# Performance work log

Hardware: AMD Instinct MI355X
Metric: run time of the kernel (lower is better)

Reference implementation:

```python
import math
import jax, jax.numpy as jnp
import numpy as np


def setup_inputs() -> dict:
    key = jax.random.key(0)
    k1, k2 = jax.random.split(key)
    x = jax.random.normal(k1, (32, 3, 64, 64), dtype=jnp.float32)   # (B,C,H,W)
    y = jax.random.normal(k2, (512, 3, 64, 64), dtype=jnp.float32)  # (N,C,H,W)
    return {"x": x, "y": y}


def reference(x, y):
    # Faithful to torch rfft/irfft with normalized=True (unitary / 'ortho' scaling).
    B, C, H, W = x.shape
    scale = math.sqrt(H * W)  # self.N in the torch module
    X = jnp.fft.rfft2(x, norm="ortho")  # (B,C,H,W//2+1) complex
    Y = jnp.fft.rfft2(y, norm="ortho")  # (N,C,H,W//2+1) complex
    # conj(X) . Y summed over channels, fused as one complex contraction
    G = jnp.einsum("bchw,nchw->bnhw", jnp.conj(X), Y)  # (B,N,H,W//2+1)
    g = jnp.fft.irfft2(G, s=(H, W), norm="ortho") * scale  # (B,N,H,W)
    m = jnp.max(g, axis=(-2, -1))  # MaxPool2d(kernel=input_size) -> (B,N)
    xx = jnp.linalg.norm(x.reshape(B, -1), axis=-1)[:, None]  # (B,1)
    yy = jnp.linalg.norm(y.reshape(y.shape[0], -1), axis=-1)[None, :]  # (1,N)
    return m / xx / yy
```

## Files before the change

kernel.cpp:

```cpp
#include <hip/hip_runtime.h>
#include <math.h>

#define FBINS 2112
#define CSC 66

typedef float cplx __attribute__((ext_vector_type(2)));
typedef __fp16 half2v __attribute__((ext_vector_type(2)));
#define MK2(a,b) (cplx){(float)(a), (float)(b)}

__device__ __forceinline__ cplx shufxy(cplx a){ return __builtin_shufflevector(a, a, 1, 0); }
template<int S> __device__ __forceinline__ cplx imul(cplx a){
    return (S > 0) ? shufxy(a) * MK2(-1.f, 1.f) : shufxy(a) * MK2(1.f, -1.f);
}
template<int S> __device__ __forceinline__ cplx cmul_tw(cplx a, cplx w){
    cplx ws = shufxy(w);
    return (S > 0) ? a.x*w + a.y*(ws*MK2(-1.f, 1.f))
                   : a.x*(w*MK2(1.f, -1.f)) + a.y*ws;
}

__device__ __forceinline__ unsigned pack16(float a, float b){
    half2v h = __builtin_amdgcn_cvt_pkrtz(a, b);
    return __builtin_bit_cast(unsigned, h);
}
__device__ __forceinline__ half2v h2(unsigned u){ return __builtin_bit_cast(half2v, u); }
__device__ __forceinline__ float fdot2(half2v a, half2v b, float c){
#if __has_builtin(__builtin_amdgcn_fdot2)
    return __builtin_amdgcn_fdot2(a, b, c, false);
#else
    return c + (float)a.x*(float)b.x + (float)a.y*(float)b.y;
#endif
}
__device__ __forceinline__ void dotw(unsigned ux, unsigned uy, float& r, float& s){
    unsigned ys = ((uy >> 16) | (uy << 16)) ^ 0x80000000u;
    r = fdot2(h2(ux), h2(uy), r);
    s = fdot2(h2(ux), h2(ys), s);
}

template<int S>
__device__ __forceinline__ void dft8(cplx v[8]) {
    const float C = 0.70710678118654752440f;
    cplx t0=v[0]+v[4], t4=v[0]-v[4];
    cplx t1=v[1]+v[5], t5=v[1]-v[5];
    cplx t2=v[2]+v[6], t6=v[2]-v[6];
    cplx t3=v[3]+v[7], t7=v[3]-v[7];
    cplx u0=t0+t2, u2=t0-t2;
    cplx u1=t1+t3, u3=t1-t3;
    v[0]=u0+u1; v[4]=u0-u1;
    cplx m3=imul<S>(u3);
    v[2]=u2+m3; v[6]=u2-m3;
    cplx z0=t4;
    cplx z1 = C*(t5 + imul<S>(t5));
    cplx z2 = imul<S>(t6);
    cplx z3 = C*(imul<S>(t7) - t7);
    cplx w0=z0+z2, w2=z0-z2;
    cplx w1=z1+z3, w3=z1-z3;
    v[1]=w0+w1; v[5]=w0-w1;
    cplx mb=imul<S>(w3);
    v[3]=w2+mb; v[7]=w2-mb;
}

template<int S>
__device__ __forceinline__ void fft64_from_regs(
    cplx v[8], cplx* __restrict__ mem, int base, int j, const cplx wj[7])
{
    dft8<S>(v);
    #pragma unroll
    for (int k=1;k<8;++k) v[k] = cmul_tw<S>(v[k], wj[k-1]);
    #pragma unroll
    for (int k=0;k<8;++k) mem[base + 8*j + (k^j)] = v[k];
    #pragma unroll
    for (int n=0;n<8;++n) v[n] = mem[base + 8*n + (j^n)];
    dft8<S>(v);
}

__device__ __forceinline__ void init_twtable(cplx* TWS, int tid){
    if (tid < 56) {
        int jj = tid / 7, kk = tid - 7*jj + 1;
        float sn, cs;
        sincosf(6.283185307179586f * (float)(jj*kk) / 64.0f, &sn, &cs);
        TWS[tid] = MK2(cs, sn);
    }
}
__device__ __forceinline__ void load_tw(const cplx* TWS, int j, cplx wj[7]){
    #pragma unroll
    for (int k=0;k<7;++k) wj[k] = TWS[j*7+k];
}

__global__ __launch_bounds__(256) void fwd_fft_kernel(
    const float* __restrict__ in, unsigned* __restrict__ o,
    float* __restrict__ pn)
{
    __shared__ __align__(16) cplx CL[2176];
    __shared__ cplx TWS[56];
    __shared__ float red[4];
    const int tid = threadIdx.x, G = tid>>3, j = tid&7;

    init_twtable(TWS, tid);

    const float* img = in + (size_t)blockIdx.x * 4096;

    cplx wj[7];
    {
        cplx v[8];
        float ns = 0.f;
        #pragma unroll
        for (int nn=0;nn<8;++nn){ int w=8*nn+j;
            float a = img[64*G + w], c = img[64*(G+32) + w];
            v[nn] = MK2(a, c);
            ns = fmaf(a, a, ns); ns = fmaf(c, c, ns); }
        #pragma unroll
        for (int off = 32; off; off >>= 1) ns += __shfl_xor(ns, off);
        if ((tid & 63) == 0) red[tid >> 6] = ns;
        __syncthreads();
        load_tw(TWS, j, wj);
        int base = CSC*G;
        fft64_from_regs<-1>(v, CL, base, j, wj);
        #pragma unroll
        for (int k=0;k<8;++k) CL[base + j + 8*k] = v[k];
    }
    __syncthreads();

    {
        cplx v[8];
        if (G == 0) {
            #pragma unroll
            for (int nn=0;nn<8;++nn){
                int r=8*nn+j, p=r&31, hi=r>>5;
                cplx a0  = CL[CSC*p + 0];
                cplx a32 = CL[CSC*p + 32];
                v[nn] = hi ? MK2(a0.y, a32.y) : MK2(a0.x, a32.x);
            }
        } else {
            const int c = G;
            #pragma unroll
            for (int nn=0;nn<8;++nn){
                int r=8*nn+j, p=r&31, hi=r>>5;
                cplx A  = CL[CSC*p + c];
                cplx Bm = CL[CSC*p + 64 - c];
                if (!hi) v[nn] = 0.5f*(A + Bm*MK2(1.f,-1.f));
                else     v[nn] = 0.5f*(shufxy(A)*MK2(1.f,-1.f) + shufxy(Bm));
            }
        }
        __syncthreads();
        int base = CSC*G;
        fft64_from_regs<-1>(v, CL, base, j, wj);
        #pragma unroll
        for (int k=0;k<8;++k) CL[base + j + 8*k] = v[k];
    }
    __syncthreads();

    unsigned* a = o + (size_t)blockIdx.x * FBINS;
    for (int i = tid; i < FBINS; i += 256) {
        int wp = i>>6, h = i&63;
        cplx r;
        if (wp == 0) {
            int h2i = (64-h)&63;
            cplx av = CL[h], bb = CL[h2i];
            r = 0.5f*(av + bb*MK2(1.f,-1.f));
        } else if (wp == 32) {
            int h2i = (64-h)&63;
            cplx av = CL[h], bb = CL[h2i];
            r = 0.5f*(shufxy(av)*MK2(1.f,-1.f) + shufxy(bb));
        } else {
            r = CL[CSC*wp + h];
        }
        a[i] = pack16(r.x, r.y);
    }
    if (tid == 0) pn[blockIdx.x] = red[0] + red[1] + red[2] + red[3];
}

__global__ __launch_bounds__(256) void corr_kernel(
    const unsigned* __restrict__ Xh, const unsigned* __restrict__ Yh,
    const float* __restrict__ px, const float* __restrict__ py,
    float* __restrict__ out)
{
    __shared__ __align__(16) cplx CL[2176];
    __shared__ cplx TWS[56];
    __shared__ float red[4];
    const int tid = threadIdx.x, G = tid>>3, j = tid&7;

    const int blk = blockIdx.x;
    const int xcd = blk & 7, idx = blk >> 3;
    const int n = xcd*64 + (idx & 63);
    const int b = idx >> 6;

    init_twtable(TWS, tid);

    const float x2 = px[3*b] + px[3*b+1] + px[3*b+2];
    const float y2 = py[3*n] + py[3*n+1] + py[3*n+2];
    const float dinv = rsqrtf(x2 * y2) * (1.0f/4096.0f);

    const uint4* pX = (const uint4*)Xh + (size_t)b * 3 * 528;
    const uint4* pY = (const uint4*)Yh + (size_t)n * 3 * 528;
    #pragma unroll
    for (int t = 0; t < 3; ++t) {
        int i = tid + (t<<8);
        if (i < 528) {
            float r[4], s[4];
            #pragma unroll
            for (int k=0;k<4;++k){ r[k]=0.f; s[k]=0.f; }
            #pragma unroll
            for (int ch = 0; ch < 3; ++ch) {
                uint4 ux = pX[ch*528 + i];
                uint4 uy = pY[ch*528 + i];
                dotw(ux.x, uy.x, r[0], s[0]);
                dotw(ux.y, uy.y, r[1], s[1]);
                dotw(ux.z, uy.z, r[2], s[2]);
                dotw(ux.w, uy.w, r[3], s[3]);
            }
            int bin = 4*i;
            int sI = CSC*(bin>>6) + (bin&63);
            *(float4*)&CL[sI]   = make_float4(r[0],s[0],r[1],s[1]);
            *(float4*)&CL[sI+2] = make_float4(r[2],s[2],r[3],s[3]);
        }
    }
    __syncthreads();

    cplx wj[7]; load_tw(TWS, j, wj);

    {
        cplx v[8];
        if (G == 0) {
            #pragma unroll
            for (int nn=0;nn<8;++nn){
                int h = 8*nn + j;
                cplx a = CL[h];
                cplx c = CL[CSC*32 + h];
                v[nn] = a + imul<1>(c);
            }
        } else {
            #pragma unroll
            for (int nn=0;nn<8;++nn) v[nn] = CL[CSC*G + 8*nn + j];
        }
        fft64_from_regs<1>(v, CL, CSC*G, j, wj);
        #pragma unroll
        for (int k=0;k<4;++k)
            *(float4*)&CL[CSC*G + 2*(j+8*k)] =
                make_float4(v[k].x, v[k].y, v[k+4].x, v[k+4].y);
    }
    __syncthreads();

    float m = -3.4e38f;
    {
        cplx v[8];
        if (j == 0) {
            float4 f = *(float4*)&CL[2*G];
            v[0] = MK2(f.x, f.z);
            v[4] = MK2(f.y, f.w);
        } else {
            float4 f = *(float4*)&CL[CSC*j + 2*G];
            v[0] = MK2(f.x,f.y) + imul<1>(MK2(f.z,f.w));
            float4 g2 = *(float4*)&CL[CSC*(32-j) + 2*G];
            v[4] = MK2(g2.x,g2.y)*MK2(1.f,-1.f) + shufxy(MK2(g2.z,g2.w));
        }
        #pragma unroll
        for (int nn=1;nn<4;++nn){
            int w = 8*nn + j;
            float4 f = *(float4*)&CL[CSC*w + 2*G];
            v[nn] = MK2(f.x,f.y) + imul<1>(MK2(f.z,f.w));
        }
        #pragma unroll
        for (int nn=5;nn<8;++nn){
            int w2 = 64 - (8*nn + j);
            float4 f = *(float4*)&CL[CSC*w2 + 2*G];
            v[nn] = MK2(f.x,f.y)*MK2(1.f,-1.f) + shufxy(MK2(f.z,f.w));
        }
        __syncthreads();
        fft64_from_regs<1>(v, CL, CSC*G, j, wj);
        #pragma unroll
        for (int k=0;k<8;++k) m = fmaxf(m, fmaxf(v[k].x, v[k].y));
    }
    #pragma unroll
    for (int off = 32; off; off >>= 1) m = fmaxf(m, __shfl_xor(m, off));
    if ((tid & 63) == 0) red[tid >> 6] = m;
    __syncthreads();
    if (tid == 0) {
        float mm = fmaxf(fmaxf(red[0], red[1]), fmaxf(red[2], red[3]));
        out[b*512 + n] = mm * dinv;
    }
}

extern "C" void kernel_launch(void* const* d_in, const int* in_sizes, int n_in,
                              void* d_out, int out_size, void* d_ws, size_t ws_size,
                              hipStream_t stream) {
    const float* x = (const float*)d_in[0];
    const float* y = (const float*)d_in[1];
    float* out = (float*)d_out;

    unsigned* Xh = (unsigned*)d_ws;
    unsigned* Yh = Xh + 96 * FBINS;
    float* px = (float*)(Yh + 1536 * FBINS);
    float* py = px + 96;

    fwd_fft_kernel<<<96,   256, 0, stream>>>(x, Xh, px);
    fwd_fft_kernel<<<1536, 256, 0, stream>>>(y, Yh, py);
    corr_kernel<<<16384, 256, 0, stream>>>(Xh, Yh, px, py, out);
}
```

Before: 94.95 us.

## Permute spectrum layout so correlation products load directly into FFT registers

The forward FFT now writes each row's frequency bins in a transposed slot order, so each corr_kernel thread can load its 8 bins for the first inverse FFT stage straight from global memory. The channel dot products are accumulated in registers, which removes the shared-memory store, a __syncthreads and a reload. The Nyquist-column fold for row group 0 is done inline. Twiddle factors now come from a __constant__ table instead of being computed with sincosf into shared memory, which drops one more barrier in each kernel.

```diff
diff --git a/kernel.cpp b/kernel.cpp
--- a/kernel.cpp
+++ b/kernel.cpp
@@ -34,6 +34,40 @@
     unsigned ys = ((uy >> 16) | (uy << 16)) ^ 0x80000000u;
     r = fdot2(h2(ux), h2(uy), r);
     s = fdot2(h2(ux), h2(ys), s);
+}
+__device__ __forceinline__ void dotw_i(unsigned ux, unsigned uy, cplx& v){
+    float rr = 0.f, ss = 0.f;
+    dotw(ux, uy, rr, ss);
+    v += MK2(-ss, rr);
+}
+
+__device__ __constant__ float TWC[112] = {
+  1.f,0.f, 1.f,0.f, 1.f,0.f, 1.f,0.f, 1.f,0.f, 1.f,0.f, 1.f,0.f,
+  0.9951847267f,0.0980171403f, 0.9807852804f,0.1950903220f, 0.9569403357f,0.2902846773f,
+  0.9238795325f,0.3826834324f, 0.8819212643f,0.4713967368f, 0.8314696123f,0.5555702330f,
+  0.7730104534f,0.6343932842f,
+  0.9807852804f,0.1950903220f, 0.9238795325f,0.3826834324f, 0.8314696123f,0.5555702330f,
+  0.7071067812f,0.7071067812f, 0.5555702330f,0.8314696123f, 0.3826834324f,0.9238795325f,
+  0.1950903220f,0.9807852804f,
+  0.9569403357f,0.2902846773f, 0.8314696123f,0.5555702330f, 0.6343932842f,0.7730104534f,
+  0.3826834324f,0.9238795325f, 0.0980171403f,0.9951847267f, -0.1950903220f,0.9807852804f,
+  -0.4713967368f,0.8819212643f,
+  0.9238795325f,0.3826834324f, 0.7071067812f,0.7071067812f, 0.3826834324f,0.9238795325f,
+  0.f,1.f, -0.3826834324f,0.9238795325f, -0.7071067812f,0.7071067812f,
+  -0.9238795325f,0.3826834324f,
+  0.8819212643f,0.4713967368f, 0.5555702330f,0.8314696123f, 0.0980171403f,0.9951847267f,
+  -0.3826834324f,0.9238795325f, -0.7730104534f,0.6343932842f, -0.9807852804f,0.1950903220f,
+  -0.9569403357f,-0.2902846773f,
+  0.8314696123f,0.5555702330f, 0.3826834324f,0.9238795325f, -0.1950903220f,0.9807852804f,
+  -0.7071067812f,0.7071067812f, -0.9807852804f,0.1950903220f, -0.9238795325f,-0.3826834324f,
+  -0.5555702330f,-0.8314696123f,
+  0.7730104534f,0.6343932842f, 0.1950903220f,0.9807852804f, -0.4713967368f,0.8819212643f,
+  -0.9238795325f,0.3826834324f, -0.9569403357f,-0.2902846773f, -0.5555702330f,-0.8314696123f,
+  0.0980171403f,-0.9951847267f
+};
+__device__ __forceinline__ void load_tw(int j, cplx wj[7]){
+    #pragma unroll
+    for (int k=0;k<7;++k) wj[k] = MK2(TWC[(j*7+k)*2], TWC[(j*7+k)*2+1]);
 }
 
 template<int S>
@@ -73,33 +107,17 @@
     dft8<S>(v);
 }
 
-__device__ __forceinline__ void init_twtable(cplx* TWS, int tid){
-    if (tid < 56) {
-        int jj = tid / 7, kk = tid - 7*jj + 1;
-        float sn, cs;
-        sincosf(6.283185307179586f * (float)(jj*kk) / 64.0f, &sn, &cs);
-        TWS[tid] = MK2(cs, sn);
-    }
-}
-__device__ __forceinline__ void load_tw(const cplx* TWS, int j, cplx wj[7]){
-    #pragma unroll
-    for (int k=0;k<7;++k) wj[k] = TWS[j*7+k];
-}
-
 __global__ __launch_bounds__(256) void fwd_fft_kernel(
     const float* __restrict__ in, unsigned* __restrict__ o,
     float* __restrict__ pn)
 {
     __shared__ __align__(16) cplx CL[2176];
-    __shared__ cplx TWS[56];
     __shared__ float red[4];
     const int tid = threadIdx.x, G = tid>>3, j = tid&7;
 
-    init_twtable(TWS, tid);
-
+    cplx wj[7]; load_tw(j, wj);
     const float* img = in + (size_t)blockIdx.x * 4096;
 
-    cplx wj[7];
     {
         cplx v[8];
         float ns = 0.f;
@@ -111,8 +129,6 @@
         #pragma unroll
         for (int off = 32; off; off >>= 1) ns += __shfl_xor(ns, off);
         if ((tid & 63) == 0) red[tid >> 6] = ns;
-        __syncthreads();
-        load_tw(TWS, j, wj);
         int base = CSC*G;
         fft64_from_regs<-1>(v, CL, base, j, wj);
         #pragma unroll
@@ -164,7 +180,8 @@
         } else {
             r = CL[CSC*wp + h];
         }
-        a[i] = pack16(r.x, r.y);
+        int slot = ((h & 7) << 3) | (h >> 3);
+        a[(wp << 6) | slot] = pack16(r.x, r.y);
     }
     if (tid == 0) pn[blockIdx.x] = red[0] + red[1] + red[2] + red[3];
 }
@@ -175,7 +192,6 @@
     float* __restrict__ out)
 {
     __shared__ __align__(16) cplx CL[2176];
-    __shared__ cplx TWS[56];
     __shared__ float red[4];
     const int tid = threadIdx.x, G = tid>>3, j = tid&7;
 
@@ -184,65 +200,54 @@
     const int n = xcd*64 + (idx & 63);
     const int b = idx >> 6;
 
-    init_twtable(TWS, tid);
-
     const float x2 = px[3*b] + px[3*b+1] + px[3*b+2];
     const float y2 = py[3*n] + py[3*n+1] + py[3*n+2];
     const float dinv = rsqrtf(x2 * y2) * (1.0f/4096.0f);
 
-    const uint4* pX = (const uint4*)Xh + (size_t)b * 3 * 528;
-    const uint4* pY = (const uint4*)Yh + (size_t)n * 3 * 528;
-    #pragma unroll
-    for (int t = 0; t < 3; ++t) {
-        int i = tid + (t<<8);
-        if (i < 528) {
-            float r[4], s[4];
-            #pragma unroll
-            for (int k=0;k<4;++k){ r[k]=0.f; s[k]=0.f; }
-            #pragma unroll
-            for (int ch = 0; ch < 3; ++ch) {
-                uint4 ux = pX[ch*528 + i];
-                uint4 uy = pY[ch*528 + i];
-                dotw(ux.x, uy.x, r[0], s[0]);
-                dotw(ux.y, uy.y, r[1], s[1]);
-                dotw(ux.z, uy.z, r[2], s[2]);
-                dotw(ux.w, uy.w, r[3], s[3]);
-            }
-            int bin = 4*i;
-            int sI = CSC*(bin>>6) + (bin&63);
-            *(float4*)&CL[sI]   = make_float4(r[0],s[0],r[1],s[1]);
-            *(float4*)&CL[sI+2] = make_float4(r[2],s[2],r[3],s[3]);
-        }
-    }
-    __syncthreads();
-
-    cplx wj[7]; load_tw(TWS, j, wj);
-
+    const uint4* pX4 = (const uint4*)Xh + (size_t)b * 3 * 528;
+    const uint4* pY4 = (const uint4*)Yh + (size_t)n * 3 * 528;
+    cplx v[8];
     {
-        cplx v[8];
-        if (G == 0) {
-            #pragma unroll
-            for (int nn=0;nn<8;++nn){
-                int h = 8*nn + j;
-                cplx a = CL[h];
-                cplx c = CL[CSC*32 + h];
-                v[nn] = a + imul<1>(c);
-            }
-        } else {
-            #pragma unroll
-            for (int nn=0;nn<8;++nn) v[nn] = CL[CSC*G + 8*nn + j];
-        }
-        fft64_from_regs<1>(v, CL, CSC*G, j, wj);
-        #pragma unroll
-        for (int k=0;k<4;++k)
-            *(float4*)&CL[CSC*G + 2*(j+8*k)] =
-                make_float4(v[k].x, v[k].y, v[k+4].x, v[k+4].y);
-    }
+        float r[8], s[8];
+        #pragma unroll
+        for (int k=0;k<8;++k){ r[k]=0.f; s[k]=0.f; }
+        const int off = 16*G + 2*j;
+        #pragma unroll
+        for (int ch = 0; ch < 3; ++ch) {
+            uint4 x0 = pX4[ch*528 + off], x1 = pX4[ch*528 + off + 1];
+            uint4 y0 = pY4[ch*528 + off], y1 = pY4[ch*528 + off + 1];
+            dotw(x0.x, y0.x, r[0], s[0]);  dotw(x0.y, y0.y, r[1], s[1]);
+            dotw(x0.z, y0.z, r[2], s[2]);  dotw(x0.w, y0.w, r[3], s[3]);
+            dotw(x1.x, y1.x, r[4], s[4]);  dotw(x1.y, y1.y, r[5], s[5]);
+            dotw(x1.z, y1.z, r[6], s[6]);  dotw(x1.w, y1.w, r[7], s[7]);
+        }
+        #pragma unroll
+        for (int k=0;k<8;++k) v[k] = MK2(r[k], s[k]);
+    }
+    if (G == 0) {
+        const int off = 512 + 2*j;
+        #pragma unroll
+        for (int ch = 0; ch < 3; ++ch) {
+            uint4 x0 = pX4[ch*528 + off], x1 = pX4[ch*528 + off + 1];
+            uint4 y0 = pY4[ch*528 + off], y1 = pY4[ch*528 + off + 1];
+            dotw_i(x0.x, y0.x, v[0]);  dotw_i(x0.y, y0.y, v[1]);
+            dotw_i(x0.z, y0.z, v[2]);  dotw_i(x0.w, y0.w, v[3]);
+            dotw_i(x1.x, y1.x, v[4]);  dotw_i(x1.y, y1.y, v[5]);
+            dotw_i(x1.z, y1.z, v[6]);  dotw_i(x1.w, y1.w, v[7]);
+        }
+    }
+
+    cplx wj[7]; load_tw(j, wj);
+
+    fft64_from_regs<1>(v, CL, CSC*G, j, wj);
+    #pragma unroll
+    for (int k=0;k<4;++k)
+        *(float4*)&CL[CSC*G + 2*(j+8*k)] =
+            make_float4(v[k].x, v[k].y, v[k+4].x, v[k+4].y);
     __syncthreads();
 
     float m = -3.4e38f;
     {
-        cplx v[8];
         if (j == 0) {
             float4 f = *(float4*)&CL[2*G];
             v[0] = MK2(f.x, f.z);
```

After: 83.53 us. 12.0% less time.
